# Performance work log

Measured on AMD Instinct MI355X. Metric: run time of the kernel, lower is better.

## Reference

```python
import jax, jax.numpy as jnp
import numpy as np
from jax import lax

B, S, E, H = 4, 1024, 512, 8
D = E // H


def setup_inputs() -> dict:
    key = jax.random.key(0)
    k1, k2, k3 = jax.random.split(key, 3)
    source = jax.random.normal(k1, (B, S, E), dtype=jnp.float32)
    target = jax.random.normal(k2, (B, S, E), dtype=jnp.float32)
    # orthogonal-initialized positional encoder [1, H, 1, D]; random rows are a fine stand-in
    enc = jax.random.normal(k3, (1, H, 1, D), dtype=jnp.float32)
    enc = enc / jnp.linalg.norm(enc, axis=-1, keepdims=True)
    return {
        "source": source,
        "target": target,
        "encoder": enc,
        "alpha": jnp.float32(1.0),
        "beta": jnp.float32(1.0),
        "gamma": jnp.float32(2.0),
    }


def _split_heads(x):
    b, s, e = x.shape
    return x.reshape(b, s, H, e // H).transpose(0, 2, 1, 3)  # [B,H,S,D]


def reference(source, target, encoder, alpha, beta, gamma):
    q = _split_heads(source)  # [B,H,S,D]
    k = _split_heads(target)  # [B,H,S,D]
    pe = encoder[0, :, 0, :]  # [H,D]

    # --- grammar (time) attention: sequential tanh recurrence over t ---
    def step(cc, k_t):
        # cc, k_t: [B,H,D]
        cc = jnp.tanh(cc * pe)
        out = jnp.einsum('bhsd,bhd->bhs', q, cc)  # [B,H,S]
        return k_t * cc, out  # decay_rate = 0.0

    cc0 = k[:, :, 0, :]                      # initial cumulative context
    k_ts = jnp.moveaxis(k, 2, 0)             # [S,B,H,D]
    _, outs = lax.scan(step, cc0, k_ts)      # outs: [S,B,H,S]
    grammar = jnp.moveaxis(outs, 0, 3) / jnp.sqrt(jnp.float32(D))  # [B,H,S,S]
    grammar = jax.nn.softmax(grammar, axis=-1)

    # --- semantic attention ---
    semantic = jnp.einsum('bhsd,bhtd->bhst', q, k) / 100.0  # [B,H,S,S]

    w = jax.nn.softmax((alpha * semantic + beta * grammar) / gamma, axis=-1)

    # merge_heads: [B,H,S,S] -> [B,S,H*S]
    wm = w.transpose(0, 2, 1, 3).reshape(B, S, H * S)
    # output: wm^T @ target -> [B, H*S, E]
    return jnp.matmul(wm.transpose(0, 2, 1), target)
```

## Files before the change

### kernel.cpp

```cpp
#include <hip/hip_runtime.h>
#include <hip/hip_bf16.h>
#include <stdint.h>

#define S_LEN 1024
#define E_DIM 512
#define H_NUM 8
#define D_DIM 64
#define B_NUM 4
#define BH_NUM 32

using s16x8 = __attribute__((ext_vector_type(8))) short;
using f32x4 = __attribute__((ext_vector_type(4))) float;
using us4   = __attribute__((ext_vector_type(4))) unsigned short;

static __device__ __forceinline__ unsigned short f2bf(float f) {
  __hip_bfloat16 h = __float2bfloat16(f);
  return __builtin_bit_cast(unsigned short, h);
}

#define NB_RECUR 8
#define NB_PACK  2048
#define NB_TR    512

__global__ __launch_bounds__(256) void k_prep(const float* __restrict__ src,
                                              const float* __restrict__ tgt,
                                              const float* __restrict__ enc,
                                              __hip_bfloat16* __restrict__ qb,
                                              __hip_bfloat16* __restrict__ kb,
                                              __hip_bfloat16* __restrict__ cb,
                                              __hip_bfloat16* __restrict__ tT) {
  __shared__ float tile[64][65];
  const int bid = blockIdx.x;
  const int tid = threadIdx.x;

  if (bid < NB_RECUR) {
    int g = bid * 256 + tid;
    int d = g & 63;
    int bh = g >> 6;
    int h = bh & 7;
    int b = bh >> 3;
    float pe = enc[h * D_DIM + d];
    float pe2 = 2.0f * pe;
    const float* tp = tgt + (size_t)b * S_LEN * E_DIM + h * D_DIM + d;
    __hip_bfloat16* cp = cb + (size_t)bh * S_LEN * D_DIM + d;

    constexpr int CH = 32;
    float bufA[CH], bufB[CH];
#pragma unroll
    for (int i = 0; i < CH; ++i) bufA[i] = tp[(size_t)i * E_DIM];
    float cc = bufA[0];

#pragma unroll 1
    for (int ch = 0; ch < S_LEN / CH; ch += 2) {
      if (ch + 1 < S_LEN / CH) {
#pragma unroll
        for (int i = 0; i < CH; ++i)
          bufB[i] = tp[(size_t)((ch + 1) * CH + i) * E_DIM];
      }
#pragma unroll
      for (int i = 0; i < CH; ++i) {
        float m = cc * pe2;
        float e = __expf(-fabsf(m));
        float th = __builtin_copysignf((1.0f - e) * __builtin_amdgcn_rcpf(1.0f + e), m);
        cp[(size_t)(ch * CH + i) * D_DIM] = __float2bfloat16(th);
        cc = bufA[i] * th;
      }
      if (ch + 2 < S_LEN / CH) {
#pragma unroll
        for (int i = 0; i < CH; ++i)
          bufA[i] = tp[(size_t)((ch + 2) * CH + i) * E_DIM];
      }
#pragma unroll
      for (int i = 0; i < CH; ++i) {
        float m = cc * pe2;
        float e = __expf(-fabsf(m));
        float th = __builtin_copysignf((1.0f - e) * __builtin_amdgcn_rcpf(1.0f + e), m);
        cp[(size_t)((ch + 1) * CH + i) * D_DIM] = __float2bfloat16(th);
        cc = bufB[i] * th;
      }
    }
  } else if (bid < NB_RECUR + NB_PACK) {
    size_t i4 = ((size_t)(bid - NB_RECUR) * 256 + tid) * 4;
    float4 s4 = *reinterpret_cast<const float4*>(src + i4);
    float4 t4 = *reinterpret_cast<const float4*>(tgt + i4);
    int e = (int)(i4 & 511);
    size_t bs = i4 >> 9;
    int s = (int)(bs & 1023);
    int b = (int)(bs >> 10);
    int h = e >> 6, d = e & 63;
    size_t o = (((size_t)(b * H_NUM + h) * S_LEN) + s) * D_DIM + d;
    us4 qv = {f2bf(s4.x), f2bf(s4.y), f2bf(s4.z), f2bf(s4.w)};
    us4 kv = {f2bf(t4.x), f2bf(t4.y), f2bf(t4.z), f2bf(t4.w)};
    *reinterpret_cast<us4*>(qb + o) = qv;
    *reinterpret_cast<us4*>(kb + o) = kv;
  } else {
    int lb = bid - (NB_RECUR + NB_PACK);
    int sx = lb & 15, ey = (lb >> 4) & 7, b = lb >> 7;
    int e0 = ey * 64, s0 = sx * 64;
    int tx = tid & 63, ty = tid >> 6;
    const float* p = tgt + ((size_t)b * S_LEN + s0) * E_DIM + e0;
#pragma unroll
    for (int r = ty; r < 64; r += 4) tile[r][tx] = p[(size_t)r * E_DIM + tx];
    __syncthreads();
    __hip_bfloat16* q = tT + ((size_t)b * E_DIM + e0) * S_LEN + s0;
#pragma unroll
    for (int r = ty; r < 64; r += 4) q[(size_t)r * S_LEN + tx] = __float2bfloat16(tile[tx][r]);
  }
}

__global__ __launch_bounds__(256) void k_weights(const __hip_bfloat16* __restrict__ qb,
                                                 const __hip_bfloat16* __restrict__ kb,
                                                 const __hip_bfloat16* __restrict__ cb,
                                                 __hip_bfloat16* __restrict__ wt,
                                                 const float* __restrict__ pal,
                                                 const float* __restrict__ pbe,
                                                 const float* __restrict__ pga) {
  __shared__ float red0[4][16];
  __shared__ float red1[4][16];

  const int tid = threadIdx.x;
  const int wave = tid >> 6, lane = tid & 63;
  const int quad = lane >> 4, col = lane & 15;
  const int bh = blockIdx.y;
  const int s0 = blockIdx.x * 16;

  const float alpha = pal[0], beta = pbe[0];
  const float inv_gamma = 1.0f / pga[0];
  const float sa = alpha * 0.01f * inv_gamma;
  const float sb = beta * inv_gamma;

  const __hip_bfloat16* qrow = qb + ((size_t)bh * S_LEN + s0 + col) * D_DIM;
  s16x8 a0 = *reinterpret_cast<const s16x8*>(qrow + quad * 8);
  s16x8 a1 = *reinterpret_cast<const s16x8*>(qrow + 32 + quad * 8);

  const int t_base = wave * 256;
  float st[16][4];

  const __hip_bfloat16* cbh = cb + ((size_t)bh * S_LEN + t_base + col) * D_DIM;
  float lg[4] = {0.f, 0.f, 0.f, 0.f};
#pragma unroll
  for (int it = 0; it < 16; ++it) {
    const __hip_bfloat16* crow = cbh + (size_t)it * 16 * D_DIM;
    s16x8 b0 = *reinterpret_cast<const s16x8*>(crow + quad * 8);
    s16x8 b1 = *reinterpret_cast<const s16x8*>(crow + 32 + quad * 8);
    f32x4 dacc = {0.f, 0.f, 0.f, 0.f};
    dacc = __builtin_amdgcn_mfma_f32_16x16x32_bf16(a0, b0, dacc, 0, 0, 0);
    dacc = __builtin_amdgcn_mfma_f32_16x16x32_bf16(a1, b1, dacc, 0, 0, 0);
#pragma unroll
    for (int i = 0; i < 4; ++i) {
      float g = __expf(dacc[i] * 0.125f);
      st[it][i] = g;
      lg[i] += g;
    }
  }
#pragma unroll
  for (int m = 1; m < 16; m <<= 1) {
#pragma unroll
    for (int i = 0; i < 4; ++i) lg[i] += __shfl_xor(lg[i], m);
  }
  if (col == 0) {
#pragma unroll
    for (int i = 0; i < 4; ++i) red0[wave][quad * 4 + i] = lg[i];
  }
  __syncthreads();
  float ilg[4];
#pragma unroll
  for (int i = 0; i < 4; ++i) {
    int r = quad * 4 + i;
    ilg[i] = 1.0f / (red0[0][r] + red0[1][r] + red0[2][r] + red0[3][r]);
  }

  const __hip_bfloat16* kbh = kb + ((size_t)bh * S_LEN + t_base + col) * D_DIM;
  float lw[4] = {0.f, 0.f, 0.f, 0.f};
#pragma unroll
  for (int it = 0; it < 16; ++it) {
    const __hip_bfloat16* krow = kbh + (size_t)it * 16 * D_DIM;
    s16x8 b0 = *reinterpret_cast<const s16x8*>(krow + quad * 8);
    s16x8 b1 = *reinterpret_cast<const s16x8*>(krow + 32 + quad * 8);
    f32x4 dacc = {0.f, 0.f, 0.f, 0.f};
    dacc = __builtin_amdgcn_mfma_f32_16x16x32_bf16(a0, b0, dacc, 0, 0, 0);
    dacc = __builtin_amdgcn_mfma_f32_16x16x32_bf16(a1, b1, dacc, 0, 0, 0);
#pragma unroll
    for (int i = 0; i < 4; ++i) {
      float z = sa * dacc[i] + sb * (st[it][i] * ilg[i]);
      float wv = __expf(z);
      st[it][i] = wv;
      lw[i] += wv;
    }
  }
#pragma unroll
  for (int m = 1; m < 16; m <<= 1) {
#pragma unroll
    for (int i = 0; i < 4; ++i) lw[i] += __shfl_xor(lw[i], m);
  }
  if (col == 0) {
#pragma unroll
    for (int i = 0; i < 4; ++i) red1[wave][quad * 4 + i] = lw[i];
  }
  __syncthreads();
  float ilw[4];
#pragma unroll
  for (int i = 0; i < 4; ++i) {
    int r = quad * 4 + i;
    ilw[i] = 1.0f / (red1[0][r] + red1[1][r] + red1[2][r] + red1[3][r]);
  }

  __hip_bfloat16* wrow = wt + ((size_t)bh * S_LEN + t_base + col) * S_LEN + s0 + quad * 4;
#pragma unroll
  for (int it = 0; it < 16; ++it) {
    us4 o;
#pragma unroll
    for (int i = 0; i < 4; ++i) o[i] = f2bf(st[it][i] * ilw[i]);
    *reinterpret_cast<us4*>(wrow + (size_t)it * 16 * S_LEN) = o;
  }
}

typedef const __attribute__((address_space(1))) uint32_t gas_uint;
typedef __attribute__((address_space(3))) uint32_t las_uint;

__global__ __launch_bounds__(256) void k_outgemm(const __hip_bfloat16* __restrict__ wt,
                                                 const __hip_bfloat16* __restrict__ tT,
                                                 float* __restrict__ out) {
  __shared__ __hip_bfloat16 As[128 * 64];
  __shared__ __hip_bfloat16 Bs[128 * 64];
  const int tid = threadIdx.x;
  const int wave = tid >> 6, lane = tid & 63;
  const int quad = lane >> 4, col = lane & 15;

  const int g = blockIdx.x;
  const int xcd = g & 7;
  const int local = g >> 3;
  const int strip = xcd * 32 + (local >> 2);
  const int ntile = local & 3;
  const int bh = strip >> 3;
  const int mt = strip & 7;
  const int b = bh >> 3;
  const int m0 = mt * 128;
  const int n0 = ntile * 128;

  const __hip_bfloat16* Ag = wt + (size_t)bh * S_LEN * S_LEN;
  const __hip_bfloat16* Bg = tT + (size_t)b * E_DIM * S_LEN;
  const int mw = (wave >> 1) * 64, nw = (wave & 1) * 64;
  const int lrow = lane >> 3;
  const int lcol = (lane & 7) * 8;

  f32x4 acc[4][4];
#pragma unroll
  for (int i = 0; i < 4; ++i)
#pragma unroll
    for (int j = 0; j < 4; ++j) acc[i][j] = (f32x4){0.f, 0.f, 0.f, 0.f};

  for (int kt = 0; kt < 16; ++kt) {
    const int k0 = kt * 64;
    __syncthreads();
#pragma unroll
    for (int j = 0; j < 4; ++j) {
      int row = j * 32 + wave * 8 + lrow;
      const __hip_bfloat16* gp = Ag + (size_t)(m0 + row) * S_LEN + k0 + lcol;
      __builtin_amdgcn_global_load_lds((gas_uint*)gp,
                                       (las_uint*)(As + (j * 32 + wave * 8) * 64),
                                       16, 0, 0);
    }
#pragma unroll
    for (int j = 0; j < 4; ++j) {
      int row = j * 32 + wave * 8 + lrow;
      const __hip_bfloat16* gp = Bg + (size_t)(n0 + row) * S_LEN + k0 + lcol;
      __builtin_amdgcn_global_load_lds((gas_uint*)gp,
                                       (las_uint*)(Bs + (j * 32 + wave * 8) * 64),
                                       16, 0, 0);
    }
    __syncthreads();
#pragma unroll
    for (int ks = 0; ks < 2; ++ks) {
      s16x8 af[4], bf[4];
#pragma unroll
      for (int i = 0; i < 4; ++i)
        af[i] = *reinterpret_cast<const s16x8*>(As + (mw + i * 16 + col) * 64 + ks * 32 + quad * 8);
#pragma unroll
      for (int i = 0; i < 4; ++i)
        bf[i] = *reinterpret_cast<const s16x8*>(Bs + (nw + i * 16 + col) * 64 + ks * 32 + quad * 8);
#pragma unroll
      for (int mi = 0; mi < 4; ++mi)
#pragma unroll
        for (int ni = 0; ni < 4; ++ni)
          acc[mi][ni] = __builtin_amdgcn_mfma_f32_16x16x32_bf16(af[mi], bf[ni], acc[mi][ni], 0, 0, 0);
    }
  }

#pragma unroll
  for (int mi = 0; mi < 4; ++mi)
#pragma unroll
    for (int ni = 0; ni < 4; ++ni)
#pragma unroll
      for (int i = 0; i < 4; ++i) {
        int m = m0 + mw + mi * 16 + quad * 4 + i;
        int n = n0 + nw + ni * 16 + col;
        out[((size_t)bh * S_LEN + m) * E_DIM + n] = acc[mi][ni][i];
      }
}

extern "C" void kernel_launch(void* const* d_in, const int* in_sizes, int n_in,
                              void* d_out, int out_size, void* d_ws, size_t ws_size,
                              hipStream_t stream) {
  (void)in_sizes; (void)n_in; (void)out_size; (void)ws_size;
  const float* src = (const float*)d_in[0];
  const float* tgt = (const float*)d_in[1];
  const float* enc = (const float*)d_in[2];
  const float* pal = (const float*)d_in[3];
  const float* pbe = (const float*)d_in[4];
  const float* pga = (const float*)d_in[5];
  float* out = (float*)d_out;

  char* ws = (char*)d_ws;
  __hip_bfloat16* qb = (__hip_bfloat16*)(ws);
  __hip_bfloat16* kb = (__hip_bfloat16*)(ws + ((size_t)4 << 20));
  __hip_bfloat16* cb = (__hip_bfloat16*)(ws + ((size_t)8 << 20));
  __hip_bfloat16* tT = (__hip_bfloat16*)(ws + ((size_t)12 << 20));
  __hip_bfloat16* wt = (__hip_bfloat16*)(ws + ((size_t)16 << 20));

  k_prep<<<NB_RECUR + NB_PACK + NB_TR, 256, 0, stream>>>(src, tgt, enc, qb, kb, cb, tT);
  k_weights<<<dim3(S_LEN / 16, BH_NUM), 256, 0, stream>>>(qb, kb, cb, wt, pal, pbe, pga);
  k_outgemm<<<dim3((E_DIM / 128) * (S_LEN / 128) * BH_NUM), 256, 0, stream>>>(wt, tT, out);
}
```

Before: 248.6 us.

## Fuse grammar and semantic score passes, store grammar scores as bf16, XCD-swizzle weights grid

The weights kernel now computes both the grammar (cb) and semantic (kb) MFMA dot products in one loop before the first reduction. The grammar exponentials are kept as packed bf16 pairs in registers, and the raw semantic scores are kept in fp32, so the second pass needs no global loads or MFMAs. The grid is flattened to 1D and remapped so that each XCD handles a contiguous set of 4 heads, which should improve L2 locality for the cb/kb/qb rows. The cost is more register pressure, possible lower occupancy, and bf16 rounding of the grammar softmax numerators.

```diff
diff --git a/kernel.cpp b/kernel.cpp
--- a/kernel.cpp
+++ b/kernel.cpp
@@ -16,6 +16,9 @@
 static __device__ __forceinline__ unsigned short f2bf(float f) {
   __hip_bfloat16 h = __float2bfloat16(f);
   return __builtin_bit_cast(unsigned short, h);
+}
+static __device__ __forceinline__ float bf2f(unsigned short u) {
+  return __bfloat162float(__builtin_bit_cast(__hip_bfloat16, u));
 }
 
 #define NB_RECUR 8
@@ -121,8 +124,12 @@
   const int tid = threadIdx.x;
   const int wave = tid >> 6, lane = tid & 63;
   const int quad = lane >> 4, col = lane & 15;
-  const int bh = blockIdx.y;
-  const int s0 = blockIdx.x * 16;
+
+  const int g = blockIdx.x;
+  const int xcd = g & 7;
+  const int r = g >> 3;
+  const int bh = xcd * 4 + (r >> 6);
+  const int s0 = (r & 63) * 16;
 
   const float alpha = pal[0], beta = pbe[0];
   const float inv_gamma = 1.0f / pga[0];
@@ -134,24 +141,38 @@
   s16x8 a1 = *reinterpret_cast<const s16x8*>(qrow + 32 + quad * 8);
 
   const int t_base = wave * 256;
-  float st[16][4];
+  uint32_t stg[16][2];
+  float    stk[16][4];
 
   const __hip_bfloat16* cbh = cb + ((size_t)bh * S_LEN + t_base + col) * D_DIM;
+  const __hip_bfloat16* kbh = kb + ((size_t)bh * S_LEN + t_base + col) * D_DIM;
   float lg[4] = {0.f, 0.f, 0.f, 0.f};
 #pragma unroll
   for (int it = 0; it < 16; ++it) {
     const __hip_bfloat16* crow = cbh + (size_t)it * 16 * D_DIM;
-    s16x8 b0 = *reinterpret_cast<const s16x8*>(crow + quad * 8);
-    s16x8 b1 = *reinterpret_cast<const s16x8*>(crow + 32 + quad * 8);
-    f32x4 dacc = {0.f, 0.f, 0.f, 0.f};
-    dacc = __builtin_amdgcn_mfma_f32_16x16x32_bf16(a0, b0, dacc, 0, 0, 0);
-    dacc = __builtin_amdgcn_mfma_f32_16x16x32_bf16(a1, b1, dacc, 0, 0, 0);
+    const __hip_bfloat16* krow = kbh + (size_t)it * 16 * D_DIM;
+    s16x8 cb0 = *reinterpret_cast<const s16x8*>(crow + quad * 8);
+    s16x8 cb1 = *reinterpret_cast<const s16x8*>(crow + 32 + quad * 8);
+    s16x8 kb0 = *reinterpret_cast<const s16x8*>(krow + quad * 8);
+    s16x8 kb1 = *reinterpret_cast<const s16x8*>(krow + 32 + quad * 8);
+    f32x4 dg = {0.f, 0.f, 0.f, 0.f};
+    dg = __builtin_amdgcn_mfma_f32_16x16x32_bf16(a0, cb0, dg, 0, 0, 0);
+    dg = __builtin_amdgcn_mfma_f32_16x16x32_bf16(a1, cb1, dg, 0, 0, 0);
+    f32x4 dk = {0.f, 0.f, 0.f, 0.f};
+    dk = __builtin_amdgcn_mfma_f32_16x16x32_bf16(a0, kb0, dk, 0, 0, 0);
+    dk = __builtin_amdgcn_mfma_f32_16x16x32_bf16(a1, kb1, dk, 0, 0, 0);
+    uint32_t p0 = 0, p1 = 0;
 #pragma unroll
     for (int i = 0; i < 4; ++i) {
-      float g = __expf(dacc[i] * 0.125f);
-      st[it][i] = g;
-      lg[i] += g;
-    }
+      float gv = __expf(dg[i] * 0.125f);
+      unsigned short u = f2bf(gv);
+      lg[i] += bf2f(u);
+      if (i < 2) p0 |= (uint32_t)u << (16 * i);
+      else       p1 |= (uint32_t)u << (16 * (i - 2));
+      stk[it][i] = dk[i];
+    }
+    stg[it][0] = p0;
+    stg[it][1] = p1;
   }
 #pragma unroll
   for (int m = 1; m < 16; m <<= 1) {
@@ -166,25 +187,21 @@
   float ilg[4];
 #pragma unroll
   for (int i = 0; i < 4; ++i) {
-    int r = quad * 4 + i;
-    ilg[i] = 1.0f / (red0[0][r] + red0[1][r] + red0[2][r] + red0[3][r]);
-  }
-
-  const __hip_bfloat16* kbh = kb + ((size_t)bh * S_LEN + t_base + col) * D_DIM;
+    int rr = quad * 4 + i;
+    ilg[i] = 1.0f / (red0[0][rr] + red0[1][rr] + red0[2][rr] + red0[3][rr]);
+  }
+
   float lw[4] = {0.f, 0.f, 0.f, 0.f};
 #pragma unroll
   for (int it = 0; it < 16; ++it) {
-    const __hip_bfloat16* krow = kbh + (size_t)it * 16 * D_DIM;
-    s16x8 b0 = *reinterpret_cast<const s16x8*>(krow + quad * 8);
-    s16x8 b1 = *reinterpret_cast<const s16x8*>(krow + 32 + quad * 8);
-    f32x4 dacc = {0.f, 0.f, 0.f, 0.f};
-    dacc = __builtin_amdgcn_mfma_f32_16x16x32_bf16(a0, b0, dacc, 0, 0, 0);
-    dacc = __builtin_amdgcn_mfma_f32_16x16x32_bf16(a1, b1, dacc, 0, 0, 0);
 #pragma unroll
     for (int i = 0; i < 4; ++i) {
-      float z = sa * dacc[i] + sb * (st[it][i] * ilg[i]);
+      unsigned short u = (unsigned short)((i < 2 ? stg[it][0] >> (16 * i)
+                                                 : stg[it][1] >> (16 * (i - 2))) & 0xffffu);
+      float gv = bf2f(u) * ilg[i];
+      float z = sa * stk[it][i] + sb * gv;
       float wv = __expf(z);
-      st[it][i] = wv;
+      stk[it][i] = wv;
       lw[i] += wv;
     }
   }
@@ -201,8 +218,8 @@
   float ilw[4];
 #pragma unroll
   for (int i = 0; i < 4; ++i) {
-    int r = quad * 4 + i;
-    ilw[i] = 1.0f / (red1[0][r] + red1[1][r] + red1[2][r] + red1[3][r]);
+    int rr = quad * 4 + i;
+    ilw[i] = 1.0f / (red1[0][rr] + red1[1][rr] + red1[2][rr] + red1[3][rr]);
   }
 
   __hip_bfloat16* wrow = wt + ((size_t)bh * S_LEN + t_base + col) * S_LEN + s0 + quad * 4;
@@ -210,7 +227,7 @@
   for (int it = 0; it < 16; ++it) {
     us4 o;
 #pragma unroll
-    for (int i = 0; i < 4; ++i) o[i] = f2bf(st[it][i] * ilw[i]);
+    for (int i = 0; i < 4; ++i) o[i] = f2bf(stk[it][i] * ilw[i]);
     *reinterpret_cast<us4*>(wrow + (size_t)it * 16 * S_LEN) = o;
   }
 }
@@ -319,6 +336,6 @@
   __hip_bfloat16* wt = (__hip_bfloat16*)(ws + ((size_t)16 << 20));
 
   k_prep<<<NB_RECUR + NB_PACK + NB_TR, 256, 0, stream>>>(src, tgt, enc, qb, kb, cb, tT);
-  k_weights<<<dim3(S_LEN / 16, BH_NUM), 256, 0, stream>>>(qb, kb, cb, wt, pal, pbe, pga);
+  k_weights<<<dim3((S_LEN / 16) * BH_NUM), 256, 0, stream>>>(qb, kb, cb, wt, pal, pbe, pga);
   k_outgemm<<<dim3((E_DIM / 128) * (S_LEN / 128) * BH_NUM), 256, 0, stream>>>(wt, tT, out);
 }
```

New measurement: 245.9 us. No clear change (-1.1%).
